# Kernel optimization log

Measured on AMD Instinct MI355X. Metric: run time of the kernel, lower is better.

## Reference

```python
import jax, jax.numpy as jnp
from jax import lax
import numpy as np


@jax.custom_vjp
def entmax15(x):
    return _entmax15_val(x)


def _entmax15_val(x):
    # 1.5-entmax along last axis (Peters et al. 2019), exact sort-based threshold
    x = (x - jnp.max(x, -1, keepdims=True)) / 2.0
    d = x.shape[-1]
    xs = -jnp.sort(-x, axis=-1)                      # descending
    rho = jnp.arange(1, d + 1, dtype=x.dtype)
    mean = jnp.cumsum(xs, -1) / rho
    mean_sq = jnp.cumsum(xs * xs, -1) / rho
    ss = rho * (mean_sq - mean * mean)
    delta = (1.0 - ss) / rho
    tau = mean - jnp.sqrt(jnp.clip(delta, 0.0))
    support = jnp.sum(tau <= xs, -1)
    tau_star = jnp.take_along_axis(tau, (support - 1)[..., None], -1)
    return jnp.square(jnp.clip(x - tau_star, 0.0))


def _entmax15_f(x):
    y = _entmax15_val(x)
    return y, y


def _entmax15_b(y, g):
    gppr = jnp.sqrt(y)                               # y^{2-alpha} with alpha=1.5
    dx = g * gppr
    q = jnp.sum(dx, -1, keepdims=True) / jnp.sum(gppr, -1, keepdims=True)
    return (dx - q * gppr,)


entmax15.defvjp(_entmax15_f, _entmax15_b)


def causal_conv(x, w, b, dilation):
    # x: [N, C_in, L]; left-pad (k-1)*dilation == conv+Chomp1d of the torch TCN
    pad = (w.shape[-1] - 1) * dilation
    y = lax.conv_general_dilated(x, w, (1,), [(pad, 0)], rhs_dilation=(dilation,),
                                 dimension_numbers=('NCH', 'OIH', 'NCH'))
    return y + b[None, :, None]


def temporal_block(x, w1, b1, w2, b2, wd, bd, dilation):
    h = jax.nn.relu(causal_conv(x, w1, b1, dilation))
    h = jax.nn.relu(causal_conv(h, w2, b2, dilation))
    res = x if wd is None else causal_conv(x, wd, bd, 1)  # 1x1 downsample
    return jax.nn.relu(h + res)


def _forward(src_seq, trg_seq,
             tcn0_w1, tcn0_b1, tcn0_w2, tcn0_b2, tcn0_wd, tcn0_bd,
             tcn1_w1, tcn1_b1, tcn1_w2, tcn1_b2,
             tcn2_w1, tcn2_b1, tcn2_w2, tcn2_b2,
             head1_w, head1_b, head2_w, head2_b):
    B, Ls, D = src_seq.shape
    Tp = trg_seq.shape[1]
    W = Ls + 1                                          # window = predict_start+1
    srctrg = jnp.concatenate([src_seq, trg_seq], axis=1)  # [B, Ls+Tp, D]
    # vectorized version of the python loop building in_conv (order: t-major, then batch)
    idx = jnp.arange(Tp)[:, None] + jnp.arange(W)[None, :]  # [Tp, W]
    win = srctrg[:, idx, :]                              # [B, Tp, W, D]
    x = win.transpose(1, 0, 3, 2).reshape(Tp * B, D, W)  # [N, D, W]
    x = temporal_block(x, tcn0_w1, tcn0_b1, tcn0_w2, tcn0_b2, tcn0_wd, tcn0_bd, 1)
    x = temporal_block(x, tcn1_w1, tcn1_b1, tcn1_w2, tcn1_b2, None, None, 2)
    x = temporal_block(x, tcn2_w1, tcn2_b1, tcn2_w2, tcn2_b2, None, None, 4)
    out = x.transpose(0, 2, 1)                           # [N, W, C]
    q = out[:, -1, :]                                    # [N, C]
    kv = out[:, :-1, :]                                  # [N, W-1, C]
    score = entmax15(jnp.einsum('nc,nlc->nl', q, kv))    # sparse attention weights
    c = jnp.einsum('nl,nlc->nc', score, kv)
    cc = jnp.concatenate([c, q], axis=-1)                # [N, 2C]
    y_hat = (cc @ head1_w.T + head1_b).reshape(Tp, B).T  # [B, Tp]
    sigma = jax.nn.softplus((cc @ head2_w.T + head2_b).reshape(Tp, B).T)
    return y_hat, sigma


def setup_inputs() -> dict:
    key = jax.random.key(0)
    ks = jax.random.split(key, 20)
    B, Ls, Tp, D, C, K = 128, 168, 24, 64, 128, 3
    n = lambda k, s: jax.random.normal(k, s, jnp.float32) * 0.05
    return {
        'src_seq': jax.random.normal(ks[0], (B, Ls, D), jnp.float32),
        'trg_seq': jax.random.normal(ks[1], (B, Tp, D), jnp.float32),
        'tcn0_w1': n(ks[2], (C, D, K)), 'tcn0_b1': n(ks[3], (C,)),
        'tcn0_w2': n(ks[4], (C, C, K)), 'tcn0_b2': n(ks[5], (C,)),
        'tcn0_wd': n(ks[6], (C, D, 1)), 'tcn0_bd': n(ks[7], (C,)),
        'tcn1_w1': n(ks[8], (C, C, K)), 'tcn1_b1': n(ks[9], (C,)),
        'tcn1_w2': n(ks[10], (C, C, K)), 'tcn1_b2': n(ks[11], (C,)),
        'tcn2_w1': n(ks[12], (C, C, K)), 'tcn2_b1': n(ks[13], (C,)),
        'tcn2_w2': n(ks[14], (C, C, K)), 'tcn2_b2': n(ks[15], (C,)),
        'head1_w': n(ks[16], (1, 2 * C)), 'head1_b': n(ks[17], (1,)),
        'head2_w': n(ks[18], (1, 2 * C)), 'head2_b': n(ks[19], (1,)),
    }


def reference(src_seq, trg_seq,
              tcn0_w1, tcn0_b1, tcn0_w2, tcn0_b2, tcn0_wd, tcn0_bd,
              tcn1_w1, tcn1_b1, tcn1_w2, tcn1_b2,
              tcn2_w1, tcn2_b1, tcn2_w2, tcn2_b2,
              head1_w, head1_b, head2_w, head2_b):
    return _forward(src_seq, trg_seq,
                    tcn0_w1, tcn0_b1, tcn0_w2, tcn0_b2, tcn0_wd, tcn0_bd,
                    tcn1_w1, tcn1_b1, tcn1_w2, tcn1_b2,
                    tcn2_w1, tcn2_b1, tcn2_w2, tcn2_b2,
                    head1_w, head1_b, head2_w, head2_b)
```

## Files before the change

kernel.cpp:

```cpp
#include <hip/hip_runtime.h>
#include <math.h>

typedef _Float16 f16;
typedef __attribute__((ext_vector_type(8))) _Float16 half8;
typedef __attribute__((ext_vector_type(2))) _Float16 half2v;
typedef __attribute__((ext_vector_type(4))) float f32x4;
typedef __attribute__((ext_vector_type(4))) float f4;

#define TPQ 24
#define BQ 128
#define LSQ 168

#if __has_builtin(__builtin_amdgcn_fdot2)
#define HAS_FDOT2 1
#else
#define HAS_FDOT2 0
#endif

#define E0 0
#define ED 24576
#define E1 32768
#define E2 81920
#define E3 131072
#define E4 180224
#define E5 229376
#define WTOT 278528
#define OG2 278528
#define OG1 2899968
#define OG0 3817472

#define MFMA16(a, b, c) __builtin_amdgcn_mfma_f32_16x16x32_f16((a), (b), (c), 0, 0, 0)

extern "C" __global__ void pack_weights(
    const float* __restrict__ w01, const float* __restrict__ wd0,
    const float* __restrict__ w02, const float* __restrict__ w11,
    const float* __restrict__ w12, const float* __restrict__ w21,
    const float* __restrict__ w22, f16* __restrict__ ws)
{
    int e = blockIdx.x * 256 + threadIdx.x;
    if (e >= WTOT) return;
    const float* W; int CIN, KK, el;
    if (e < ED) { W = w01; CIN = 64; KK = 3; el = e; }
    else if (e < E1) { W = wd0; CIN = 64; KK = 1; el = e - ED; }
    else {
        int c = (e - E1) / 49152; el = (e - E1) % 49152; CIN = 128; KK = 3;
        W = (c == 0) ? w02 : (c == 1) ? w11 : (c == 2) ? w12 : (c == 3) ? w21 : w22;
    }
    const int KB = CIN / 32;
    const int frag = el >> 9, wi = el & 511, lane = wi >> 3, i = wi & 7;
    const int coT = frag / (KK * KB), rem = frag % (KK * KB);
    const int kk = rem / KB, kb = rem % KB;
    const int co = coT * 16 + (lane & 15);
    const int ci = kb * 32 + (lane >> 4) * 8 + i;
    ws[e] = (f16)W[(co * CIN + ci) * KK + kk];
}

template<int CIN, int KK, int DIL, int RES, int RELU>
__device__ __forceinline__ void phaseA(
    const char* __restrict__ inb, char* __restrict__ outb,
    const f16* __restrict__ ws, int eoff, const float* __restrict__ bias, int tid)
{
    constexpr int KB = CIN / 32;
    constexpr int RB = CIN * 2;
    const int lane = tid & 63, wid = tid >> 6;
    const int cg = wid & 3, wg = wid >> 2;
    const int colr = lane & 15, quad = lane >> 4;
    const half8* __restrict__ wp = (const half8*)(ws + eoff);
    half8 wf[2][KK][KB];
#pragma unroll
    for (int ct = 0; ct < 2; ++ct)
#pragma unroll
        for (int kk = 0; kk < KK; ++kk)
#pragma unroll
            for (int kb = 0; kb < KB; ++kb)
                wf[ct][kk][kb] = wp[((((cg * 2 + ct) * KK) + kk) * KB + kb) * 64 + lane];
    const float bv0 = bias[cg * 32 + colr], bv1 = bias[cg * 32 + 16 + colr];
    const int t0 = wg ? 3 : 0, t1 = wg ? 5 : 3;
    for (int t = t0; t < t1; ++t) {
        const int w = t * 16 + colr;
        f32x4 a0 = {0.f, 0.f, 0.f, 0.f}, a1 = {0.f, 0.f, 0.f, 0.f};
#pragma unroll
        for (int kk = 0; kk < KK; ++kk) {
            const int r8 = w + 8 - (KK - 1 - kk) * DIL;
            const int rb = r8 * RB, sx = r8 & 7;
#pragma unroll
            for (int kb = 0; kb < KB; ++kb) {
                const half8 a = *(const half8*)(inb + rb + ((((kb * 4 + quad) ^ sx)) << 4));
                a0 = MFMA16(a, wf[0][kk][kb], a0);
                a1 = MFMA16(a, wf[1][kk][kb], a1);
            }
        }
#pragma unroll
        for (int ct = 0; ct < 2; ++ct) {
            const float bv = ct ? bv1 : bv0;
            const int co = cg * 32 + ct * 16 + colr;
#pragma unroll
            for (int j = 0; j < 4; ++j) {
                const int r8o = t * 16 + quad * 4 + j + 8;
                char* p = outb + r8o * 256 + ((((co >> 3) ^ (r8o & 7))) << 4) + ((co & 7) << 1);
                float v = (ct ? a1[j] : a0[j]) + bv;
                if (RELU) v = fmaxf(v, 0.f);
                if (RES)  v = fmaxf(v + (float)*(const f16*)p, 0.f);
                *(f16*)p = (f16)v;
            }
        }
    }
}

extern "C" __global__ void __launch_bounds__(512, 2)
tcn_global(const float* __restrict__ src, const float* __restrict__ trg,
           f16* __restrict__ ws,
           const float* __restrict__ b01, const float* __restrict__ bd0,
           const float* __restrict__ b02, const float* __restrict__ b11,
           const float* __restrict__ b12, const float* __restrict__ b21,
           const float* __restrict__ b22)
{
    __shared__ __align__(16) char sX[88 * 128];
    __shared__ __align__(16) char sH1[88 * 256];
    __shared__ __align__(16) char sH2[88 * 256];
    const int tid = threadIdx.x;
    const int b = blockIdx.x >> 2, chunk = blockIdx.x & 3;
    const int u0 = chunk * 48;
    const float* srcb = src + (size_t)b * LSQ * 64;
    const float* trgb = trg + (size_t)b * TPQ * 64;

    for (int e = tid; e < 80 * 8; e += 512) {
        const int w = e >> 3, gg = e & 7;
        const int p = u0 - 28 + w;
        half8 v = {};
        if (p >= 0 && p < 192) {
            const float* ptr = (p < 168) ? (srcb + p * 64 + gg * 8) : (trgb + (p - 168) * 64 + gg * 8);
            const f4 f0 = *(const f4*)ptr; const f4 f1 = *(const f4*)(ptr + 4);
            v[0] = (f16)f0[0]; v[1] = (f16)f0[1]; v[2] = (f16)f0[2]; v[3] = (f16)f0[3];
            v[4] = (f16)f1[0]; v[5] = (f16)f1[1]; v[6] = (f16)f1[2]; v[7] = (f16)f1[3];
        }
        const int r8 = w + 8;
        *(half8*)(sX + r8 * 128 + ((gg ^ (r8 & 7)) << 4)) = v;
    }
    if (tid < 320) {
        const half8 z = {};
        if (tid < 64)       *(half8*)(sX + tid * 16) = z;
        else if (tid < 192) *(half8*)(sH1 + (tid - 64) * 16) = z;
        else                *(half8*)(sH2 + (tid - 192) * 16) = z;
    }
    __syncthreads();

    phaseA<64, 3, 1, 0, 1>(sX, sH1, ws, E0, b01, tid);
    phaseA<64, 1, 1, 0, 0>(sX, sH2, ws, ED, bd0, tid);
    __syncthreads();
    phaseA<128, 3, 1, 1, 1>(sH1, sH2, ws, E1, b02, tid);
    __syncthreads();
    phaseA<128, 3, 2, 0, 1>(sH2, sH1, ws, E2, b11, tid);
    if (chunk == 0) {
        for (int e = tid; e < 40 * 16; e += 512) {
            const int p = e >> 4, gc = e & 15, r8 = p + 36;
            const half8 v = *(const half8*)(sH2 + r8 * 256 + ((gc ^ (r8 & 7)) << 4));
            *(half8*)(ws + OG0 + (size_t)(b * 40 + p) * 128 + gc * 8) = v;
        }
    }
    __syncthreads();
    phaseA<128, 3, 2, 1, 1>(sH1, sH2, ws, E3, b12, tid);
    __syncthreads();
    phaseA<128, 3, 4, 0, 1>(sH2, sH1, ws, E4, b21, tid);
    if (chunk == 0) {
        for (int e = tid; e < 48 * 16; e += 512) {
            const int p = e >> 4, gc = e & 15, r8 = p + 36;
            const half8 v = *(const half8*)(sH2 + r8 * 256 + ((gc ^ (r8 & 7)) << 4));
            *(half8*)(ws + OG1 + (size_t)(b * 56 + p) * 128 + gc * 8) = v;
        }
    } else if (chunk == 1) {
        for (int e = tid; e < 8 * 16; e += 512) {
            const int p = 48 + (e >> 4), gc = e & 15, r8 = p - 12;
            const half8 v = *(const half8*)(sH2 + r8 * 256 + ((gc ^ (r8 & 7)) << 4));
            *(half8*)(ws + OG1 + (size_t)(b * 56 + p) * 128 + gc * 8) = v;
        }
    }
    __syncthreads();
    phaseA<128, 3, 4, 1, 1>(sH1, sH2, ws, E5, b22, tid);
    __syncthreads();
    for (int e = tid; e < 48 * 16; e += 512) {
        const int pl = e >> 4, gc = e & 15, r8 = pl + 36;
        const int p = u0 + pl;
        if (p >= 32) {
            const half8 v = *(const half8*)(sH2 + r8 * 256 + ((gc ^ (r8 & 7)) << 4));
            *(half8*)(ws + OG2 + (size_t)(b * 160 + (p - 32)) * 128 + gc * 8) = v;
        }
    }
}

template<int CIN, int KK, int DIL, int WPG, int SIN, int SOUT, int RES, int RELU, int NT>
__device__ __forceinline__ void bc_conv8(
    const char* __restrict__ inb, char* __restrict__ outb, const char* __restrict__ zrp,
    const f16* __restrict__ ws, int eoff, const float* __restrict__ bias, int tid)
{
    constexpr int KB = CIN / 32;
    constexpr int RB = CIN * 2;
    const int lane = tid & 63, wid = tid >> 6;
    const int colr = lane & 15, quad = lane >> 4;
    const half8* __restrict__ wp = (const half8*)(ws + eoff);
    half8 wf[KK][KB];
#pragma unroll
    for (int kk = 0; kk < KK; ++kk)
#pragma unroll
        for (int kb = 0; kb < KB; ++kb)
            wf[kk][kb] = wp[((wid * KK + kk) * KB + kb) * 64 + lane];
    const float bv = bias[wid * 16 + colr];
#pragma unroll
    for (int t = 0; t < NT; ++t) {
        const int m = t * 16 + colr;
        const int g = m / WPG, w = m - g * WPG;
        f32x4 aA = {0.f, 0.f, 0.f, 0.f}, aB = {0.f, 0.f, 0.f, 0.f};
#pragma unroll
        for (int kk = 0; kk < KK; ++kk) {
            const int wq = w - (KK - 1 - kk) * DIL;
            const int row = g * SIN + wq;
            const char* rb = (wq < 0) ? zrp : (inb + row * RB);
            const int sx = (wq < 0) ? 0 : (row & 7);
#pragma unroll
            for (int kb = 0; kb < KB; ++kb) {
                const half8 a = *(const half8*)(rb + ((((kb * 4 + quad) ^ sx)) << 4));
                if (kb & 1) aB = MFMA16(a, wf[kk][kb], aB);
                else        aA = MFMA16(a, wf[kk][kb], aA);
            }
        }
        const int co = wid * 16 + colr;
#pragma unroll
        for (int j = 0; j < 4; ++j) {
            const int mo = t * 16 + quad * 4 + j;
            const int go = mo / WPG, wo = mo - go * WPG;
            const int row = go * SOUT + wo;
            char* p = outb + row * 256 + ((((co >> 3) ^ (row & 7))) << 4) + ((co & 7) << 1);
            float v = aA[j] + aB[j] + bv;
            if (RELU) v = fmaxf(v, 0.f);
            if (RES)  v = fmaxf(v + (float)*(const f16*)p, 0.f);
            *(f16*)p = (f16)v;
        }
    }
}

__device__ __forceinline__ void bc_p2_8(
    const char* __restrict__ bx, const char* __restrict__ cb1, char* __restrict__ outB,
    const char* __restrict__ zrp, const f16* __restrict__ ws,
    const float* __restrict__ b02, const float* __restrict__ bd0, int tid)
{
    const int lane = tid & 63, wid = tid >> 6;
    const int colr = lane & 15, quad = lane >> 4;
    const half8* __restrict__ wpA = (const half8*)(ws + E1);
    const half8* __restrict__ wpD = (const half8*)(ws + ED);
    half8 wfa[3][4], wfd[2];
#pragma unroll
    for (int kk = 0; kk < 3; ++kk)
#pragma unroll
        for (int kb = 0; kb < 4; ++kb)
            wfa[kk][kb] = wpA[((wid * 3 + kk) * 4 + kb) * 64 + lane];
#pragma unroll
    for (int kb = 0; kb < 2; ++kb)
        wfd[kb] = wpD[(wid * 2 + kb) * 64 + lane];
    const float ba = b02[wid * 16 + colr];
    const float bd = bd0[wid * 16 + colr];
    const int g = colr >> 2, w = colr & 3;
    f32x4 aA = {0.f,0.f,0.f,0.f}, aB = {0.f,0.f,0.f,0.f};
    f32x4 dA = {0.f,0.f,0.f,0.f}, dB = {0.f,0.f,0.f,0.f};
#pragma unroll
    for (int kk = 0; kk < 3; ++kk) {
        const int wq = w - (2 - kk);
        const int row = g * 4 + wq;
        const char* rb = (wq < 0) ? zrp : (cb1 + row * 256);
        const int sx = (wq < 0) ? 0 : (row & 7);
#pragma unroll
        for (int kb = 0; kb < 4; ++kb) {
            const half8 a = *(const half8*)(rb + ((((kb * 4 + quad) ^ sx)) << 4));
            if (kb & 1) aB = MFMA16(a, wfa[kk][kb], aB);
            else        aA = MFMA16(a, wfa[kk][kb], aA);
        }
    }
    {
        const int row = g * 4 + w;
        const char* rb = bx + row * 128;
        const int sx = row & 7;
        const half8 x0 = *(const half8*)(rb + (((0 * 4 + quad) ^ sx) << 4));
        const half8 x1 = *(const half8*)(rb + (((1 * 4 + quad) ^ sx) << 4));
        dA = MFMA16(x0, wfd[0], dA);
        dB = MFMA16(x1, wfd[1], dB);
    }
    const int co = wid * 16 + colr;
#pragma unroll
    for (int j = 0; j < 4; ++j) {
        const int mo = quad * 4 + j;
        const int go = mo >> 2, wo = mo & 3;
        const int row = go * 32 + wo;
        char* p = outB + row * 256 + ((((co >> 3) ^ (row & 7))) << 4) + ((co & 7) << 1);
        const float ca = aA[j] + aB[j] + ba;
        const float cd = dA[j] + dB[j] + bd;
        *(f16*)p = (f16)fmaxf(fmaxf(ca, 0.f) + cd, 0.f);
    }
}

__device__ __forceinline__ float dot8(half8 kv, half8 vq, float s) {
#if HAS_FDOT2
#pragma unroll
    for (int j2 = 0; j2 < 4; ++j2) {
        half2v a = {kv[2 * j2], kv[2 * j2 + 1]};
        half2v q = {vq[2 * j2], vq[2 * j2 + 1]};
        s = __builtin_amdgcn_fdot2(a, q, s, false);
    }
#else
#pragma unroll
    for (int j = 0; j < 8; ++j) s = fmaf((float)kv[j], (float)vq[j], s);
#endif
    return s;
}

extern "C" __global__ void __launch_bounds__(512, 2)
tcn_bdattn(const float* __restrict__ src, const f16* __restrict__ ws,
           const float* __restrict__ b01, const float* __restrict__ bd0,
           const float* __restrict__ b02, const float* __restrict__ b11,
           const float* __restrict__ b12, const float* __restrict__ b21,
           const float* __restrict__ b22,
           const float* __restrict__ h1w, const float* __restrict__ h1b,
           const float* __restrict__ h2w, const float* __restrict__ h2b,
           float* __restrict__ out)
{
    __shared__ __align__(16) char BufB[128 * 256];
    __shared__ __align__(16) char BufC[128 * 256];
    __shared__ __align__(16) char zr[256];
    __shared__ __align__(16) f16 qh[512];
    __shared__ float qf[512];
    __shared__ float sc[672];
    __shared__ float xs[672];
    __shared__ float cvp[2][4][128];
    char* scb1 = BufC;
    char* sbx  = BufC + 4096;

    const int tid = threadIdx.x, lane = tid & 63, wid = tid >> 6;
    const int n0 = blockIdx.x << 2;
    const int tp = n0 >> 7, b0 = n0 & 127;

    if (tid < 16) *(half8*)(zr + tid * 16) = half8{};
    if (tid < 128) {
        const int g = tid >> 5, w = (tid >> 3) & 3, gg = tid & 7;
        const float* ptr = src + ((size_t)(b0 + g) * LSQ + (tp + w)) * 64 + gg * 8;
        const f4 f0 = *(const f4*)ptr; const f4 f1 = *(const f4*)(ptr + 4);
        half8 v;
        v[0] = (f16)f0[0]; v[1] = (f16)f0[1]; v[2] = (f16)f0[2]; v[3] = (f16)f0[3];
        v[4] = (f16)f1[0]; v[5] = (f16)f1[1]; v[6] = (f16)f1[2]; v[7] = (f16)f1[3];
        const int row = g * 4 + w;
        *(half8*)(sbx + row * 128 + ((gg ^ (row & 7)) << 4)) = v;
    }
    for (int e = tid; e < 768; e += 512) {
        const int gc = e & 15, q = e >> 4;
        const int g = q / 12, pw = 4 + (q - g * 12);
        const half8 v = *(const half8*)(ws + OG0 + (size_t)((b0 + g) * 40 + (tp + pw)) * 128 + gc * 8);
        const int row = g * 32 + pw;
        *(half8*)(BufB + row * 256 + ((gc ^ (row & 7)) << 4)) = v;
    }
    for (int e = tid; e < 1024; e += 512) {
        const int gc = e & 15, q = e >> 4;
        const int g = q >> 4, pw = 16 + (q & 15);
        const half8 v = *(const half8*)(ws + OG1 + (size_t)((b0 + g) * 56 + (tp + pw)) * 128 + gc * 8);
        const int row = g * 32 + pw;
        *(half8*)(BufB + row * 256 + ((gc ^ (row & 7)) << 4)) = v;
    }
    if (tid < 64) {
        const int g = tid >> 4, gc = tid & 15;
        const half8 v = *(const half8*)(ws + OG2 + ((size_t)(b0 + g) * 160 + tp + 136) * 128 + gc * 8);
        *(half8*)(qh + g * 128 + gc * 8) = v;
#pragma unroll
        for (int j = 0; j < 8; ++j) qf[g * 128 + gc * 8 + j] = (float)v[j];
    }
    __syncthreads();

    bc_conv8<64, 3, 1, 4, 4, 4, 0, 1, 1>(sbx, scb1, zr, ws, E0, b01, tid);
    __syncthreads();
    bc_p2_8(sbx, scb1, BufB, zr, ws, b02, bd0, tid);
    __syncthreads();
    bc_conv8<128, 3, 2, 16, 32, 32, 0, 1, 4>(BufB, BufC, zr, ws, E2, b11, tid);
    __syncthreads();
    bc_conv8<128, 3, 2, 16, 32, 32, 1, 1, 4>(BufC, BufB, zr, ws, E3, b12, tid);
    __syncthreads();
    bc_conv8<128, 3, 4, 32, 32, 32, 0, 1, 8>(BufB, BufC, zr, ws, E4, b21, tid);
    __syncthreads();
    bc_conv8<128, 3, 4, 32, 32, 32, 1, 1, 8>(BufC, BufB, zr, ws, E5, b22, tid);
    __syncthreads();

    const int g = wid >> 1, h = wid & 1;
    const int b = b0 + g;
    const f16* __restrict__ g2r = ws + OG2 + ((size_t)b * 160 + tp - 32) * 128;
    const int wbase = h * 84;

#pragma unroll
    for (int it = 0; it < 2; ++it) {
        const int w = wbase + it * 64 + lane;
        if (it == 0 || lane < 20) {
            float s = 0.f;
            if (w < 32) {
                const int row = g * 32 + w, sx = row & 7;
                const char* rb = BufB + row * 256;
#pragma unroll
                for (int gc = 0; gc < 16; ++gc) {
                    const half8 kv = *(const half8*)(rb + ((gc ^ sx) << 4));
                    const half8 vq = *(const half8*)(qh + g * 128 + gc * 8);
                    s = dot8(kv, vq, s);
                }
            } else {
                const half8* rb = (const half8*)(g2r + (size_t)w * 128);
#pragma unroll
                for (int gc = 0; gc < 16; ++gc) {
                    const half8 kv = rb[gc];
                    const half8 vq = *(const half8*)(qh + g * 128 + gc * 8);
                    s = dot8(kv, vq, s);
                }
            }
            sc[g * 168 + w] = s;
        }
    }
    __syncthreads();

    {
        const int w0i = wbase + lane;
        const int w1i = wbase + 64 + lane;
        const float v0 = sc[g * 168 + w0i];
        const float v1 = (lane < 20) ? sc[g * 168 + w1i] : 0.f;
        int r0 = 0, r1 = 0;
        for (int m2 = 0; m2 < LSQ; ++m2) {
            const float u = sc[g * 168 + m2];
            r0 += (u > v0) || ((u == v0) && (m2 < w0i));
            r1 += (u > v1) || ((u == v1) && (m2 < w1i));
        }
        xs[g * 168 + r0] = v0;
        if (lane < 20) xs[g * 168 + r1] = v1;
    }
    __syncthreads();

    const float mx = xs[g * 168];
    float tau;
    {
        const int i0 = lane * 3;
        const float a0 = (i0     < LSQ) ? (xs[g * 168 + i0]     - mx) * 0.5f : 0.f;
        const float a1 = (i0 + 1 < LSQ) ? (xs[g * 168 + i0 + 1] - mx) * 0.5f : 0.f;
        const float a2 = (i0 + 2 < LSQ) ? (xs[g * 168 + i0 + 2] - mx) * 0.5f : 0.f;
        const float s1 = a0, s2 = a0 + a1, s3 = a0 + a1 + a2;
        const float q1 = a0 * a0, q2 = q1 + a1 * a1, q3 = q2 + a2 * a2;
        float ts = s3, tq = q3;
#pragma unroll
        for (int o = 1; o < 64; o <<= 1) {
            const float us = __shfl_up(ts, o);
            const float uq = __shfl_up(tq, o);
            if (lane >= o) { ts += us; tq += uq; }
        }
        const float eS = ts - s3, eQ = tq - q3;
        float tau0v, tau1v, tau2v; int ind = 0;
#define TAUC(CIDX, CS, CQ, AV, TVAR) { \
        const float rho = (float)(i0 + CIDX + 1); \
        const float mean = (CS) / rho; \
        const float msq = (CQ) / rho; \
        const float ssv = rho * (msq - mean * mean); \
        float delta = (1.f - ssv) / rho; \
        delta = delta > 0.f ? delta : 0.f; \
        TVAR = mean - sqrtf(delta); \
        if (i0 + CIDX < LSQ && TVAR <= (AV)) ++ind; }
        TAUC(0, eS + s1, eQ + q1, a0, tau0v)
        TAUC(1, eS + s2, eQ + q2, a1, tau1v)
        TAUC(2, eS + s3, eQ + q3, a2, tau2v)
#undef TAUC
#pragma unroll
        for (int o = 32; o; o >>= 1) ind += __shfl_xor(ind, o);
        const int sm1 = ind - 1;
        const int srcl = sm1 / 3, c = sm1 - srcl * 3;
        const float tsel = (c == 0) ? tau0v : (c == 1) ? tau1v : tau2v;
        tau = __shfl(tsel, srcl);
    }

    {
        const int c0 = lane * 2;
        float cv0 = 0.f, cv1 = 0.f;
#pragma unroll 4
        for (int wi = 0; wi < 84; ++wi) {
            const int w = wbase + wi;
            float pz = (sc[g * 168 + w] - mx) * 0.5f - tau;
            pz = fmaxf(pz, 0.f);
            const float pw = pz * pz;
            float k0, k1;
            if (w < 32) {
                const int row = g * 32 + w, sx = row & 7;
                const char* p = BufB + row * 256 + (((c0 >> 3) ^ sx) << 4) + ((c0 & 7) << 1);
                k0 = (float)*(const f16*)p;
                k1 = (float)*(const f16*)(p + 2);
            } else {
                const f16* p = g2r + (size_t)w * 128 + c0;
                k0 = (float)p[0];
                k1 = (float)p[1];
            }
            cv0 = fmaf(pw, k0, cv0);
            cv1 = fmaf(pw, k1, cv1);
        }
        cvp[h][g][c0] = cv0;
        cvp[h][g][c0 + 1] = cv1;
    }
    __syncthreads();

    if (h == 0) {
        const int c0 = lane * 2;
        const float cva = cvp[0][g][c0]     + cvp[1][g][c0];
        const float cvb = cvp[0][g][c0 + 1] + cvp[1][g][c0 + 1];
        const float q0 = qf[g * 128 + c0], q1 = qf[g * 128 + c0 + 1];
        float s1 = h1w[c0] * cva + h1w[c0 + 1] * cvb + h1w[128 + c0] * q0 + h1w[128 + c0 + 1] * q1;
        float s2 = h2w[c0] * cva + h2w[c0 + 1] * cvb + h2w[128 + c0] * q0 + h2w[128 + c0 + 1] * q1;
#pragma unroll
        for (int o = 32; o; o >>= 1) {
            s1 += __shfl_xor(s1, o);
            s2 += __shfl_xor(s2, o);
        }
        if (lane == 0) {
            const float y1 = s1 + h1b[0];
            const float z = s2 + h2b[0];
            const float sp = (z > 0.f) ? (z + log1pf(expf(-z))) : log1pf(expf(z));
            out[b * TPQ + tp] = y1;
            out[BQ * TPQ + b * TPQ + tp] = sp;
        }
    }
}

extern "C" void kernel_launch(void* const* d_in, const int* in_sizes, int n_in,
                              void* d_out, int out_size, void* d_ws, size_t ws_size,
                              hipStream_t stream) {
    const float* src = (const float*)d_in[0];
    const float* trg = (const float*)d_in[1];
    const float* w01 = (const float*)d_in[2];
    const float* b01 = (const float*)d_in[3];
    const float* w02 = (const float*)d_in[4];
    const float* b02 = (const float*)d_in[5];
    const float* wd0 = (const float*)d_in[6];
    const float* bd0 = (const float*)d_in[7];
    const float* w11 = (const float*)d_in[8];
    const float* b11 = (const float*)d_in[9];
    const float* w12 = (const float*)d_in[10];
    const float* b12 = (const float*)d_in[11];
    const float* w21 = (const float*)d_in[12];
    const float* b21 = (const float*)d_in[13];
    const float* w22 = (const float*)d_in[14];
    const float* b22 = (const float*)d_in[15];
    const float* h1w = (const float*)d_in[16];
    const float* h1b = (const float*)d_in[17];
    const float* h2w = (const float*)d_in[18];
    const float* h2b = (const float*)d_in[19];
    f16* ws = (f16*)d_ws;

    pack_weights<<<dim3((WTOT + 255) / 256), dim3(256), 0, stream>>>(
        w01, wd0, w02, w11, w12, w21, w22, ws);

    tcn_global<<<dim3(BQ * 4), dim3(512), 0, stream>>>(
        src, trg, ws, b01, bd0, b02, b11, b12, b21, b22);

    tcn_bdattn<<<dim3(TPQ * BQ / 4), dim3(512), 0, stream>>>(
        src, ws, b01, bd0, b02, b11, b12, b21, b22,
        h1w, h1b, h2w, h2b, (float*)d_out);
}
```

Baseline: 172.3 us.

## Halve bdattn block to 256 threads with 64-channel-per-wave MFMA conv tiles

The tail kernel runs with 4 waves instead of 8. Each wave now computes 64 output channels (4 MFMA accumulators sharing one A fragment) over half the time tiles. The LDS swizzle widens from 8 to 16 rows, and the attention/entmax stage assigns one wave per batch row, which removes the cross-wave partial-sum buffer and one barrier. The intent is to reuse A-operand loads across more channels and cut LDS traffic and synchronisation. The cost is higher register pressure from 48 weight fragments per wave, launch bounds reduced to (256,1), and fewer waves to hide latency.

```diff
diff --git a/kernel.cpp b/kernel.cpp
--- a/kernel.cpp
+++ b/kernel.cpp
@@ -188,58 +188,116 @@
     }
 }
 
-template<int CIN, int KK, int DIL, int WPG, int SIN, int SOUT, int RES, int RELU, int NT>
-__device__ __forceinline__ void bc_conv8(
+template<int DIL, int WPG, int NTW, int RES>
+__device__ __forceinline__ void bc_conv64(
     const char* __restrict__ inb, char* __restrict__ outb, const char* __restrict__ zrp,
     const f16* __restrict__ ws, int eoff, const float* __restrict__ bias, int tid)
 {
-    constexpr int KB = CIN / 32;
-    constexpr int RB = CIN * 2;
+    const int lane = tid & 63, wid = tid >> 6;
+    const int ch = wid & 1;
+    const int mh = wid >> 1;
+    const int colr = lane & 15, quad = lane >> 4;
+    const half8* __restrict__ wp = (const half8*)(ws + eoff);
+    half8 wf[4][3][4];
+#pragma unroll
+    for (int ct = 0; ct < 4; ++ct)
+#pragma unroll
+        for (int kk = 0; kk < 3; ++kk)
+#pragma unroll
+            for (int kb = 0; kb < 4; ++kb)
+                wf[ct][kk][kb] = wp[((((ch * 4 + ct) * 3) + kk) * 4 + kb) * 64 + lane];
+    float bv[4];
+#pragma unroll
+    for (int ct = 0; ct < 4; ++ct) bv[ct] = bias[ch * 64 + ct * 16 + colr];
+#pragma unroll
+    for (int ti = 0; ti < NTW; ++ti) {
+        const int t = mh * NTW + ti;
+        const int m = t * 16 + colr;
+        const int g = m / WPG, w = m - g * WPG;
+        f32x4 ac0 = {0.f,0.f,0.f,0.f}, ac1 = {0.f,0.f,0.f,0.f};
+        f32x4 ac2 = {0.f,0.f,0.f,0.f}, ac3 = {0.f,0.f,0.f,0.f};
+#pragma unroll
+        for (int kk = 0; kk < 3; ++kk) {
+            const int wq = w - (2 - kk) * DIL;
+            const int row = g * 32 + wq;
+            const char* rb = (wq < 0) ? zrp : (inb + row * 256);
+            const int sx = (wq < 0) ? 0 : (row & 15);
+#pragma unroll
+            for (int kb = 0; kb < 4; ++kb) {
+                const half8 a = *(const half8*)(rb + ((((kb * 4 + quad) ^ sx)) << 4));
+                ac0 = MFMA16(a, wf[0][kk][kb], ac0);
+                ac1 = MFMA16(a, wf[1][kk][kb], ac1);
+                ac2 = MFMA16(a, wf[2][kk][kb], ac2);
+                ac3 = MFMA16(a, wf[3][kk][kb], ac3);
+            }
+        }
+#pragma unroll
+        for (int ct = 0; ct < 4; ++ct) {
+            const f32x4 av = (ct == 0) ? ac0 : (ct == 1) ? ac1 : (ct == 2) ? ac2 : ac3;
+            const int co = ch * 64 + ct * 16 + colr;
+#pragma unroll
+            for (int j = 0; j < 4; ++j) {
+                const int mo = t * 16 + quad * 4 + j;
+                const int go = mo / WPG, wo = mo - go * WPG;
+                const int row = go * 32 + wo;
+                char* p = outb + row * 256 + ((((co >> 3) ^ (row & 15))) << 4) + ((co & 7) << 1);
+                float v = fmaxf(av[j] + bv[ct], 0.f);
+                if (RES) v = fmaxf(v + (float)*(const f16*)p, 0.f);
+                *(f16*)p = (f16)v;
+            }
+        }
+    }
+}
+
+__device__ __forceinline__ void bc_c1b0(
+    const char* __restrict__ sbx, char* __restrict__ scb1, const char* __restrict__ zrp,
+    const f16* __restrict__ ws, const float* __restrict__ bias, int tid)
+{
     const int lane = tid & 63, wid = tid >> 6;
     const int colr = lane & 15, quad = lane >> 4;
-    const half8* __restrict__ wp = (const half8*)(ws + eoff);
-    half8 wf[KK][KB];
-#pragma unroll
-    for (int kk = 0; kk < KK; ++kk)
-#pragma unroll
-        for (int kb = 0; kb < KB; ++kb)
-            wf[kk][kb] = wp[((wid * KK + kk) * KB + kb) * 64 + lane];
-    const float bv = bias[wid * 16 + colr];
-#pragma unroll
-    for (int t = 0; t < NT; ++t) {
-        const int m = t * 16 + colr;
-        const int g = m / WPG, w = m - g * WPG;
-        f32x4 aA = {0.f, 0.f, 0.f, 0.f}, aB = {0.f, 0.f, 0.f, 0.f};
-#pragma unroll
-        for (int kk = 0; kk < KK; ++kk) {
-            const int wq = w - (KK - 1 - kk) * DIL;
-            const int row = g * SIN + wq;
-            const char* rb = (wq < 0) ? zrp : (inb + row * RB);
-            const int sx = (wq < 0) ? 0 : (row & 7);
-#pragma unroll
-            for (int kb = 0; kb < KB; ++kb) {
-                const half8 a = *(const half8*)(rb + ((((kb * 4 + quad) ^ sx)) << 4));
-                if (kb & 1) aB = MFMA16(a, wf[kk][kb], aB);
-                else        aA = MFMA16(a, wf[kk][kb], aA);
-            }
-        }
-        const int co = wid * 16 + colr;
+    const half8* __restrict__ wp = (const half8*)(ws + E0);
+    half8 wf[2][3][2];
+#pragma unroll
+    for (int ct = 0; ct < 2; ++ct)
+#pragma unroll
+        for (int kk = 0; kk < 3; ++kk)
+#pragma unroll
+            for (int kb = 0; kb < 2; ++kb)
+                wf[ct][kk][kb] = wp[((((wid * 2 + ct) * 3) + kk) * 2 + kb) * 64 + lane];
+    const float bv0 = bias[wid * 32 + colr], bv1 = bias[wid * 32 + 16 + colr];
+    const int g = colr >> 2, w = colr & 3;
+    f32x4 a0 = {0.f,0.f,0.f,0.f}, a1 = {0.f,0.f,0.f,0.f};
+#pragma unroll
+    for (int kk = 0; kk < 3; ++kk) {
+        const int wq = w - (2 - kk);
+        const int row = g * 4 + wq;
+        const char* rb = (wq < 0) ? zrp : (sbx + row * 128);
+        const int sx = (wq < 0) ? 0 : (row & 7);
+#pragma unroll
+        for (int kb = 0; kb < 2; ++kb) {
+            const half8 a = *(const half8*)(rb + ((((kb * 4 + quad) ^ sx)) << 4));
+            a0 = MFMA16(a, wf[0][kk][kb], a0);
+            a1 = MFMA16(a, wf[1][kk][kb], a1);
+        }
+    }
+#pragma unroll
+    for (int ct = 0; ct < 2; ++ct) {
+        const f32x4 av = ct ? a1 : a0;
+        const float bv = ct ? bv1 : bv0;
+        const int co = wid * 32 + ct * 16 + colr;
 #pragma unroll
         for (int j = 0; j < 4; ++j) {
-            const int mo = t * 16 + quad * 4 + j;
-            const int go = mo / WPG, wo = mo - go * WPG;
-            const int row = go * SOUT + wo;
-            char* p = outb + row * 256 + ((((co >> 3) ^ (row & 7))) << 4) + ((co & 7) << 1);
-            float v = aA[j] + aB[j] + bv;
-            if (RELU) v = fmaxf(v, 0.f);
-            if (RES)  v = fmaxf(v + (float)*(const f16*)p, 0.f);
-            *(f16*)p = (f16)v;
-        }
-    }
-}
-
-__device__ __forceinline__ void bc_p2_8(
-    const char* __restrict__ bx, const char* __restrict__ cb1, char* __restrict__ outB,
+            const int mo = quad * 4 + j;
+            const int go = mo >> 2, wo = mo & 3;
+            const int row = go * 4 + wo;
+            char* p = scb1 + row * 256 + ((((co >> 3) ^ (row & 15))) << 4) + ((co & 7) << 1);
+            *(f16*)p = (f16)fmaxf(av[j] + bv, 0.f);
+        }
+    }
+}
+
+__device__ __forceinline__ void bc_p2(
+    const char* __restrict__ sbx, const char* __restrict__ scb1, char* __restrict__ outB,
     const char* __restrict__ zrp, const f16* __restrict__ ws,
     const float* __restrict__ b02, const float* __restrict__ bd0, int tid)
 {
@@ -247,52 +305,60 @@
     const int colr = lane & 15, quad = lane >> 4;
     const half8* __restrict__ wpA = (const half8*)(ws + E1);
     const half8* __restrict__ wpD = (const half8*)(ws + ED);
-    half8 wfa[3][4], wfd[2];
-#pragma unroll
-    for (int kk = 0; kk < 3; ++kk)
-#pragma unroll
-        for (int kb = 0; kb < 4; ++kb)
-            wfa[kk][kb] = wpA[((wid * 3 + kk) * 4 + kb) * 64 + lane];
-#pragma unroll
-    for (int kb = 0; kb < 2; ++kb)
-        wfd[kb] = wpD[(wid * 2 + kb) * 64 + lane];
-    const float ba = b02[wid * 16 + colr];
-    const float bd = bd0[wid * 16 + colr];
+    half8 wfa[2][3][4], wfd[2][2];
+#pragma unroll
+    for (int ct = 0; ct < 2; ++ct) {
+#pragma unroll
+        for (int kk = 0; kk < 3; ++kk)
+#pragma unroll
+            for (int kb = 0; kb < 4; ++kb)
+                wfa[ct][kk][kb] = wpA[((((wid * 2 + ct) * 3) + kk) * 4 + kb) * 64 + lane];
+#pragma unroll
+        for (int kb = 0; kb < 2; ++kb)
+            wfd[ct][kb] = wpD[((wid * 2 + ct) * 2 + kb) * 64 + lane];
+    }
     const int g = colr >> 2, w = colr & 3;
-    f32x4 aA = {0.f,0.f,0.f,0.f}, aB = {0.f,0.f,0.f,0.f};
-    f32x4 dA = {0.f,0.f,0.f,0.f}, dB = {0.f,0.f,0.f,0.f};
+    f32x4 aA0 = {0.f,0.f,0.f,0.f}, aA1 = {0.f,0.f,0.f,0.f};
+    f32x4 dA0 = {0.f,0.f,0.f,0.f}, dA1 = {0.f,0.f,0.f,0.f};
 #pragma unroll
     for (int kk = 0; kk < 3; ++kk) {
         const int wq = w - (2 - kk);
         const int row = g * 4 + wq;
-        const char* rb = (wq < 0) ? zrp : (cb1 + row * 256);
-        const int sx = (wq < 0) ? 0 : (row & 7);
+        const char* rb = (wq < 0) ? zrp : (scb1 + row * 256);
+        const int sx = (wq < 0) ? 0 : (row & 15);
 #pragma unroll
         for (int kb = 0; kb < 4; ++kb) {
             const half8 a = *(const half8*)(rb + ((((kb * 4 + quad) ^ sx)) << 4));
-            if (kb & 1) aB = MFMA16(a, wfa[kk][kb], aB);
-            else        aA = MFMA16(a, wfa[kk][kb], aA);
+            aA0 = MFMA16(a, wfa[0][kk][kb], aA0);
+            aA1 = MFMA16(a, wfa[1][kk][kb], aA1);
         }
     }
     {
         const int row = g * 4 + w;
-        const char* rb = bx + row * 128;
+        const char* rb = sbx + row * 128;
         const int sx = row & 7;
-        const half8 x0 = *(const half8*)(rb + (((0 * 4 + quad) ^ sx) << 4));
-        const half8 x1 = *(const half8*)(rb + (((1 * 4 + quad) ^ sx) << 4));
-        dA = MFMA16(x0, wfd[0], dA);
-        dB = MFMA16(x1, wfd[1], dB);
-    }
-    const int co = wid * 16 + colr;
-#pragma unroll
-    for (int j = 0; j < 4; ++j) {
-        const int mo = quad * 4 + j;
-        const int go = mo >> 2, wo = mo & 3;
-        const int row = go * 32 + wo;
-        char* p = outB + row * 256 + ((((co >> 3) ^ (row & 7))) << 4) + ((co & 7) << 1);
-        const float ca = aA[j] + aB[j] + ba;
-        const float cd = dA[j] + dB[j] + bd;
-        *(f16*)p = (f16)fmaxf(fmaxf(ca, 0.f) + cd, 0.f);
+#pragma unroll
+        for (int kb = 0; kb < 2; ++kb) {
+            const half8 x = *(const half8*)(rb + ((((kb * 4 + quad) ^ sx)) << 4));
+            dA0 = MFMA16(x, wfd[0][kb], dA0);
+            dA1 = MFMA16(x, wfd[1][kb], dA1);
+        }
+    }
+#pragma unroll
+    for (int ct = 0; ct < 2; ++ct) {
+        const f32x4 av = ct ? aA1 : aA0;
+        const f32x4 dv = ct ? dA1 : dA0;
+        const int co = wid * 32 + ct * 16 + colr;
+        const float ba = b02[co];
+        const float bd = bd0[co];
+#pragma unroll
+        for (int j = 0; j < 4; ++j) {
+            const int mo = quad * 4 + j;
+            const int go = mo >> 2, wo = mo & 3;
+            const int row = go * 32 + wo;
+            char* p = outB + row * 256 + ((((co >> 3) ^ (row & 15))) << 4) + ((co & 7) << 1);
+            *(f16*)p = (f16)fmaxf(fmaxf(av[j] + ba, 0.f) + dv[j] + bd, 0.f);
+        }
     }
 }
 
@@ -311,7 +377,7 @@
     return s;
 }
 
-extern "C" __global__ void __launch_bounds__(512, 2)
+extern "C" __global__ void __launch_bounds__(256, 1)
 tcn_bdattn(const float* __restrict__ src, const f16* __restrict__ ws,
            const float* __restrict__ b01, const float* __restrict__ bd0,
            const float* __restrict__ b02, const float* __restrict__ b11,
@@ -328,7 +394,6 @@
     __shared__ float qf[512];
     __shared__ float sc[672];
     __shared__ float xs[672];
-    __shared__ float cvp[2][4][128];
     char* scb1 = BufC;
     char* sbx  = BufC + 4096;
 
@@ -347,19 +412,19 @@
         const int row = g * 4 + w;
         *(half8*)(sbx + row * 128 + ((gg ^ (row & 7)) << 4)) = v;
     }
-    for (int e = tid; e < 768; e += 512) {
+    for (int e = tid; e < 768; e += 256) {
         const int gc = e & 15, q = e >> 4;
         const int g = q / 12, pw = 4 + (q - g * 12);
         const half8 v = *(const half8*)(ws + OG0 + (size_t)((b0 + g) * 40 + (tp + pw)) * 128 + gc * 8);
         const int row = g * 32 + pw;
-        *(half8*)(BufB + row * 256 + ((gc ^ (row & 7)) << 4)) = v;
-    }
-    for (int e = tid; e < 1024; e += 512) {
+        *(half8*)(BufB + row * 256 + ((gc ^ (row & 15)) << 4)) = v;
+    }
+    for (int e = tid; e < 1024; e += 256) {
         const int gc = e & 15, q = e >> 4;
         const int g = q >> 4, pw = 16 + (q & 15);
         const half8 v = *(const half8*)(ws + OG1 + (size_t)((b0 + g) * 56 + (tp + pw)) * 128 + gc * 8);
         const int row = g * 32 + pw;
-        *(half8*)(BufB + row * 256 + ((gc ^ (row & 7)) << 4)) = v;
+        *(half8*)(BufB + row * 256 + ((gc ^ (row & 15)) << 4)) = v;
     }
     if (tid < 64) {
         const int g = tid >> 4, gc = tid & 15;
@@ -370,31 +435,30 @@
     }
     __syncthreads();
 
-    bc_conv8<64, 3, 1, 4, 4, 4, 0, 1, 1>(sbx, scb1, zr, ws, E0, b01, tid);
-    __syncthreads();
-    bc_p2_8(sbx, scb1, BufB, zr, ws, b02, bd0, tid);
-    __syncthreads();
-    bc_conv8<128, 3, 2, 16, 32, 32, 0, 1, 4>(BufB, BufC, zr, ws, E2, b11, tid);
-    __syncthreads();
-    bc_conv8<128, 3, 2, 16, 32, 32, 1, 1, 4>(BufC, BufB, zr, ws, E3, b12, tid);
-    __syncthreads();
-    bc_conv8<128, 3, 4, 32, 32, 32, 0, 1, 8>(BufB, BufC, zr, ws, E4, b21, tid);
-    __syncthreads();
-    bc_conv8<128, 3, 4, 32, 32, 32, 1, 1, 8>(BufC, BufB, zr, ws, E5, b22, tid);
-    __syncthreads();
-
-    const int g = wid >> 1, h = wid & 1;
+    bc_c1b0(sbx, scb1, zr, ws, b01, tid);
+    __syncthreads();
+    bc_p2(sbx, scb1, BufB, zr, ws, b02, bd0, tid);
+    __syncthreads();
+    bc_conv64<2, 16, 2, 0>(BufB, BufC, zr, ws, E2, b11, tid);
+    __syncthreads();
+    bc_conv64<2, 16, 2, 1>(BufC, BufB, zr, ws, E3, b12, tid);
+    __syncthreads();
+    bc_conv64<4, 32, 4, 0>(BufB, BufC, zr, ws, E4, b21, tid);
+    __syncthreads();
+    bc_conv64<4, 32, 4, 1>(BufC, BufB, zr, ws, E5, b22, tid);
+    __syncthreads();
+
+    const int g = wid;
     const int b = b0 + g;
     const f16* __restrict__ g2r = ws + OG2 + ((size_t)b * 160 + tp - 32) * 128;
-    const int wbase = h * 84;
-
-#pragma unroll
-    for (int it = 0; it < 2; ++it) {
-        const int w = wbase + it * 64 + lane;
-        if (it == 0 || lane < 20) {
+
+#pragma unroll
+    for (int it = 0; it < 3; ++it) {
+        const int w = it * 64 + lane;
+        if (it < 2 || lane < 40) {
             float s = 0.f;
             if (w < 32) {
-                const int row = g * 32 + w, sx = row & 7;
+                const int row = g * 32 + w, sx = row & 15;
                 const char* rb = BufB + row * 256;
 #pragma unroll
                 for (int gc = 0; gc < 16; ++gc) {
@@ -416,26 +480,27 @@
     }
     __syncthreads();
 
+    const int i0 = lane * 3;
     {
-        const int w0i = wbase + lane;
-        const int w1i = wbase + 64 + lane;
-        const float v0 = sc[g * 168 + w0i];
-        const float v1 = (lane < 20) ? sc[g * 168 + w1i] : 0.f;
-        int r0 = 0, r1 = 0;
+        const float v0 = (i0     < LSQ) ? sc[g * 168 + i0]     : 0.f;
+        const float v1 = (i0 + 1 < LSQ) ? sc[g * 168 + i0 + 1] : 0.f;
+        const float v2 = (i0 + 2 < LSQ) ? sc[g * 168 + i0 + 2] : 0.f;
+        int r0 = 0, r1 = 0, r2 = 0;
         for (int m2 = 0; m2 < LSQ; ++m2) {
             const float u = sc[g * 168 + m2];
-            r0 += (u > v0) || ((u == v0) && (m2 < w0i));
-            r1 += (u > v1) || ((u == v1) && (m2 < w1i));
-        }
-        xs[g * 168 + r0] = v0;
-        if (lane < 20) xs[g * 168 + r1] = v1;
+            r0 += (u > v0) || ((u == v0) && (m2 < i0));
+            r1 += (u > v1) || ((u == v1) && (m2 < i0 + 1));
+            r2 += (u > v2) || ((u == v2) && (m2 < i0 + 2));
+        }
+        if (i0     < LSQ) xs[g * 168 + r0] = v0;
+        if (i0 + 1 < LSQ) xs[g * 168 + r1] = v1;
+        if (i0 + 2 < LSQ) xs[g * 168 + r2] = v2;
     }
     __syncthreads();
 
     const float mx = xs[g * 168];
     float tau;
     {
-        const int i0 = lane * 3;
         const float a0 = (i0     < LSQ) ? (xs[g * 168 + i0]     - mx) * 0.5f : 0.f;
         const float a1 = (i0 + 1 < LSQ) ? (xs[g * 168 + i0 + 1] - mx) * 0.5f : 0.f;
         const float a2 = (i0 + 2 < LSQ) ? (xs[g * 168 + i0 + 2] - mx) * 0.5f : 0.f;
@@ -475,14 +540,13 @@
         const int c0 = lane * 2;
         float cv0 = 0.f, cv1 = 0.f;
 #pragma unroll 4
-        for (int wi = 0; wi < 84; ++wi) {
-            const int w = wbase + wi;
+        for (int w = 0; w < LSQ; ++w) {
             float pz = (sc[g * 168 + w] - mx) * 0.5f - tau;
             pz = fmaxf(pz, 0.f);
             const float pw = pz * pz;
             float k0, k1;
             if (w < 32) {
-                const int row = g * 32 + w, sx = row & 7;
+                const int row = g * 32 + w, sx = row & 15;
                 const char* p = BufB + row * 256 + (((c0 >> 3) ^ sx) << 4) + ((c0 & 7) << 1);
                 k0 = (float)*(const f16*)p;
                 k1 = (float)*(const f16*)(p + 2);
@@ -494,18 +558,9 @@
             cv0 = fmaf(pw, k0, cv0);
             cv1 = fmaf(pw, k1, cv1);
         }
-        cvp[h][g][c0] = cv0;
-        cvp[h][g][c0 + 1] = cv1;
-    }
-    __syncthreads();
-
-    if (h == 0) {
-        const int c0 = lane * 2;
-        const float cva = cvp[0][g][c0]     + cvp[1][g][c0];
-        const float cvb = cvp[0][g][c0 + 1] + cvp[1][g][c0 + 1];
         const float q0 = qf[g * 128 + c0], q1 = qf[g * 128 + c0 + 1];
-        float s1 = h1w[c0] * cva + h1w[c0 + 1] * cvb + h1w[128 + c0] * q0 + h1w[128 + c0 + 1] * q1;
-        float s2 = h2w[c0] * cva + h2w[c0 + 1] * cvb + h2w[128 + c0] * q0 + h2w[128 + c0 + 1] * q1;
+        float s1 = h1w[c0] * cv0 + h1w[c0 + 1] * cv1 + h1w[128 + c0] * q0 + h1w[128 + c0 + 1] * q1;
+        float s2 = h2w[c0] * cv0 + h2w[c0 + 1] * cv1 + h2w[128 + c0] * q0 + h2w[128 + c0 + 1] * q1;
 #pragma unroll
         for (int o = 32; o; o >>= 1) {
             s1 += __shfl_xor(s1, o);
@@ -552,7 +607,7 @@
     tcn_global<<<dim3(BQ * 4), dim3(512), 0, stream>>>(
         src, trg, ws, b01, bd0, b02, b11, b12, b21, b22);
 
-    tcn_bdattn<<<dim3(TPQ * BQ / 4), dim3(512), 0, stream>>>(
+    tcn_bdattn<<<dim3(TPQ * BQ / 4), dim3(256), 0, stream>>>(
         src, ws, b01, bd0, b02, b11, b12, b21, b22,
         h1w, h1b, h2w, h2b, (float*)d_out);
 }
```

After: 198.6 us. 1.15x slower.
